# Kernel optimization log

Measured on AMD Instinct MI355X. Metric: run time of the kernel, lower is better.

## Reference

```python
import jax, jax.numpy as jnp
import numpy as np


def setup_inputs() -> dict:
    key = jax.random.key(0)
    ks = jax.random.split(key, 8)
    B, N, F, H, D, C = 16, 8192, 512, 512, 256, 2
    s = 0.02
    return {
        "h": jax.random.normal(ks[0], (B, N, F), dtype=jnp.float32),
        "W1": jax.random.normal(ks[1], (F, H), dtype=jnp.float32) * s,
        "b1": jnp.zeros((H,), jnp.float32),
        "Wa": jax.random.normal(ks[2], (H, D), dtype=jnp.float32) * s,
        "ba": jnp.zeros((D,), jnp.float32),
        "Wb": jax.random.normal(ks[3], (H, D), dtype=jnp.float32) * s,
        "bb": jnp.zeros((D,), jnp.float32),
        "Wc": jax.random.normal(ks[4], (D, 1), dtype=jnp.float32) * s,
        "bc": jnp.zeros((1,), jnp.float32),
        "Wcls": jax.random.normal(ks[5], (H, C), dtype=jnp.float32) * s,
        "bcls": jnp.zeros((C,), jnp.float32),
    }


def reference(h, W1, b1, Wa, ba, Wb, bb, Wc, bc, Wcls, bcls):
    # h: [B, N, F]  (B bags, N instances each)
    h1 = jax.nn.relu(jnp.einsum("bnf,fh->bnh", h, W1) + b1)        # [B,N,H]
    a = jnp.tanh(jnp.einsum("bnh,hd->bnd", h1, Wa) + ba)           # [B,N,D]
    g = jax.nn.sigmoid(jnp.einsum("bnh,hd->bnd", h1, Wb) + bb)     # [B,N,D]
    A = jnp.einsum("bnd,dk->bnk", a * g, Wc) + bc                  # [B,N,1]
    A_raw = jnp.swapaxes(A, 1, 2)                                  # [B,1,N]
    A_sm = jax.nn.softmax(A_raw, axis=-1)                          # [B,1,N]
    M = jnp.einsum("bkn,bnh->bkh", A_sm, h1)                       # [B,1,H]
    context = jnp.mean(M, axis=0)                                  # [1,H]  (sum / len(h_list))
    logits = context @ Wcls + bcls                                 # [1,C]
    Y_prob = jax.nn.softmax(logits, axis=1)
    Y_hat = jnp.argmax(logits, axis=1, keepdims=True)
    return (logits, Y_prob, Y_hat, A_raw, M)
```

## Files before the change

### kernel.cpp

```cpp
#include <hip/hip_runtime.h>
#include <math.h>

typedef short bf16x8 __attribute__((ext_vector_type(8)));
typedef float f32x4  __attribute__((ext_vector_type(4)));

#define GLOAD_LDS16(SRC, DST) \
  __builtin_amdgcn_global_load_lds((const __attribute__((address_space(1))) void*)(SRC), \
      (__attribute__((address_space(3))) void*)(DST), 16, 0, 0)

#define WAITVM(N) asm volatile("s_waitcnt vmcnt(" #N ")" ::: "memory")
#define WAITLGKM0 asm volatile("s_waitcnt lgkmcnt(0)" ::: "memory")
#define BARRIER() do { __builtin_amdgcn_s_barrier(); asm volatile("" ::: "memory"); } while (0)

__device__ __forceinline__ unsigned short f2bf(float f) {
  union { float f; unsigned u; } v; v.f = f;
  unsigned r = v.u + 0x7FFFu + ((v.u >> 16) & 1u);
  return (unsigned short)(r >> 16);
}
__device__ __forceinline__ float bf2f(unsigned short s) {
  union { unsigned u; float f; } v; v.u = ((unsigned)s) << 16;
  return v.f;
}
__device__ __forceinline__ unsigned pk2bf(float lo, float hi) {
  unsigned r;
  asm("v_cvt_pk_bf16_f32 %0, %1, %2" : "=v"(r) : "v"(lo), "v"(hi));
  return r;
}
__device__ __forceinline__ float fexp2(float x) {
  float r; asm("v_exp_f32 %0, %1" : "=v"(r) : "v"(x)); return r;
}
__device__ __forceinline__ float frcp(float x) {
  float r; asm("v_rcp_f32 %0, %1" : "=v"(r) : "v"(x)); return r;
}
#define LOG2E 1.44269504f
__device__ __forceinline__ float fexp(float x) { return fexp2(x * LOG2E); }


__global__ void carp_wpack(const float* __restrict__ W1, const float* __restrict__ Wa,
                           const float* __restrict__ Wb,
                           unsigned short* __restrict__ W1T_pk, unsigned short* __restrict__ WabT_pk) {
  int t = blockIdx.x * 256 + threadIdx.x;
  int mat = t >> 15;
  int gid = t & 32767;
  int g = gid & 511;
  int kt = (gid >> 9) & 15;
  int p = gid >> 13;
  int s = g >> 6, l = g & 63;
  int k = kt * 32 + (l >> 4) * 8;
  unsigned short v[8];
  if (mat == 0) {
    int j = p * 128 + s * 16 + (l & 15);
#pragma unroll
    for (int e = 0; e < 8; ++e) v[e] = f2bf(W1[(size_t)(k + e) * 512 + j]);
    *(uint4*)(W1T_pk + (size_t)gid * 8) = *(const uint4*)v;
  } else {
    int lc = s * 16 + (l & 15);
    int d = p * 64 + (lc & 63);
    const float* Wx = (lc >> 6) ? Wb : Wa;
#pragma unroll
    for (int e = 0; e < 8; ++e) v[e] = f2bf(Wx[(size_t)(k + e) * 256 + d]);
    *(uint4*)(WabT_pk + (size_t)gid * 8) = *(const uint4*)v;
  }
}

__launch_bounds__(512, 2)
__global__ void carp_gemm1(const float* __restrict__ h, const unsigned short* __restrict__ W1T_pk,
                           const float* __restrict__ b1, unsigned short* __restrict__ h1_pk) {
  __shared__ __align__(16) unsigned short lds[65536];
  int bid0 = blockIdx.x;
  int bid = (bid0 & 7) * 128 + (bid0 >> 3);
  int bn = bid & 1, bm = bid >> 1;
  int brow = bm * 256;
  int tid = threadIdx.x, lane = tid & 63, wid = tid >> 6;
  int wr = wid >> 1, wc = wid & 1;

  f32x4 acc[4][8] = {};
  float4 ar[8];

  int r0 = tid >> 4;
  int chunk = tid & 15;
  const float* hbase = h + (size_t)(brow + r0) * 512 + chunk * 4;
  int kgA = (chunk & 7) >> 1, r16A = r0 & 15;
  int aw_const = (chunk >> 3) * 8192 + (r0 >> 4) * 1024 + kgA * 256
               + ((r16A * 16) ^ (kgA << 5) ^ ((chunk >> 3) << 4)) + (chunk & 1) * 8;
  int aread_lane = (lane >> 4) * 256 + (((lane & 15) * 16) ^ ((lane >> 4) << 5));

#define G1_LOADA(TP) do { \
  _Pragma("unroll") for (int q = 0; q < 8; ++q) \
    ar[q] = *(const float4*)(hbase + (size_t)(q * 32) * 512 + (TP) * 64); \
  } while (0)
#define G1_WRITEA(TP) do { \
  char* dstA = (char*)lds + ((TP) & 1) * 32768; \
  _Pragma("unroll") for (int q = 0; q < 8; ++q) { \
    uint2 wv; wv.x = pk2bf(ar[q].x, ar[q].y); wv.y = pk2bf(ar[q].z, ar[q].w); \
    *(uint2*)(dstA + (q >> 2) * 16384 + (q & 3) * 2048 + aw_const) = wv; \
  } } while (0)
#define G1_STAGEB(TP, BUF) do { \
  _Pragma("unroll") for (int q = 0; q < 4; ++q) { \
    int c = wid * 4 + q; \
    int pn = 2 * bn + ((c & 15) >> 3); \
    GLOAD_LDS16(W1T_pk + ((size_t)(pn * 16 + (TP) * 2 + (c >> 4)) * 512 + (c & 7) * 64 + lane) * 8, \
                (char*)lds + 65536 + (BUF) * 32768 + (size_t)c * 1024); \
  } } while (0)

  G1_LOADA(0);
  WAITVM(0);
  G1_WRITEA(0);
  G1_STAGEB(0, 0);
  G1_LOADA(1);
  WAITLGKM0;

#pragma unroll 1
  for (int tp = 0; tp < 8; ++tp) {
    if (tp < 7) G1_STAGEB(tp + 1, (tp + 1) & 1);
    if (tp < 7) { WAITVM(12); } else { WAITVM(0); }
    BARRIER();
    const char* Abase = (const char*)lds + (tp & 1) * 32768;
    const char* Bbase = (const char*)lds + 65536 + (tp & 1) * 32768;
#pragma unroll
    for (int tt = 0; tt < 2; ++tt) {
      bf16x8 afr[4], bfr[8];
#pragma unroll
      for (int m = 0; m < 4; ++m) {
        int gs = wr * 4 + m;
        afr[m] = *(const bf16x8*)(Abase + (gs >> 3) * 16384 + tt * 8192
                                  + (gs & 7) * 1024 + (aread_lane ^ (tt << 4)));
      }
#pragma unroll
      for (int n = 0; n < 8; ++n)
        bfr[n] = *(const bf16x8*)(Bbase + tt * 16384 + wc * 8192
                                  + (size_t)(n * 64 + lane) * 16);
#pragma unroll
      for (int m = 0; m < 4; ++m)
#pragma unroll
        for (int n = 0; n < 8; ++n)
          acc[m][n] = __builtin_amdgcn_mfma_f32_16x16x32_bf16(afr[m], bfr[n], acc[m][n], 0, 0, 0);
    }
    if (tp < 7) { WAITVM(4); G1_WRITEA(tp + 1); }
    if (tp < 6) G1_LOADA(tp + 2);
    WAITLGKM0;
    BARRIER();
  }
#undef G1_LOADA
#undef G1_WRITEA
#undef G1_STAGEB

  unsigned short* img = lds;
#pragma unroll
  for (int n = 0; n < 8; ++n) {
    int cl = wc * 128 + n * 16 + (lane & 15);
    float bias = b1[bn * 256 + cl];
    int ktc = cl >> 5, c32 = cl & 31;
#pragma unroll
    for (int m = 0; m < 4; ++m)
#pragma unroll
      for (int j = 0; j < 4; ++j) {
        int r = wr * 64 + m * 16 + (lane >> 4) * 4 + j;
        float v = acc[m][n][j] + bias;
        v = v > 0.f ? v : 0.f;
        int gidx = (r >> 7) * 4096 + ktc * 512 + ((r & 127) >> 4) * 64 + (c32 >> 3) * 16 + (r & 15);
        img[(size_t)gidx * 8 + (c32 & 7)] = f2bf(v);
      }
  }
  __syncthreads();
#pragma unroll
  for (int i = 0; i < 16; ++i) {
    int g = i * 512 + tid;
    int P = (2 * bm + (g >> 12)) * 16 + bn * 8 + ((g >> 9) & 7);
    *(uint4*)(h1_pk + ((size_t)P * 512 + (g & 511)) * 8) = *(const uint4*)(img + (size_t)g * 8);
  }
}

#define G2_STAGE(T32, HALF, BUF) do { \
  _Pragma("unroll") for (int q = 0; q < 2; ++q) { \
    int c = wid * 2 + q; \
    int P = (2 * bm + (c >> 3)) * 16 + (T32); \
    GLOAD_LDS16(h1_pk + ((size_t)P * 512 + (c & 7) * 64 + lane) * 8, \
                (char*)lds + (BUF) * 32768 + (HALF) * 16384 + (size_t)c * 1024); \
  } \
  _Pragma("unroll") for (int q = 0; q < 2; ++q) { \
    int c2 = wid * 2 + q; \
    int pn = 2 * bn + (c2 >> 3); \
    GLOAD_LDS16(WabT_pk + ((size_t)(pn * 16 + (T32)) * 512 + (c2 & 7) * 64 + lane) * 8, \
                (char*)lds + 65536 + (BUF) * 32768 + (HALF) * 16384 + (size_t)c2 * 1024); \
  } } while (0)

__launch_bounds__(512, 2)
__global__ void carp_gemm2(const unsigned short* __restrict__ h1_pk, const unsigned short* __restrict__ WabT_pk,
                           const float* __restrict__ ba, const float* __restrict__ bb,
                           const float* __restrict__ Wc, float* __restrict__ A_part) {
  __shared__ __align__(16) unsigned short lds[65536];
  int bid0 = blockIdx.x;
  int bid = (bid0 & 7) * 128 + (bid0 >> 3);
  int bn = bid & 1, bm = bid >> 1;
  int tid = threadIdx.x, lane = tid & 63, wid = tid >> 6;
  int wr = wid >> 1, wc = wid & 1;

  f32x4 acc[4][8] = {};

  G2_STAGE(0, 0, 0); G2_STAGE(1, 1, 0);

#pragma unroll 1
  for (int kt = 0; kt < 8; ++kt) {
    int cur = kt & 1, nxt = cur ^ 1;
    if (kt < 7) { G2_STAGE(2 * kt + 2, 0, nxt); G2_STAGE(2 * kt + 3, 1, nxt); }
    if (kt < 7) { WAITVM(8); } else { WAITVM(0); }
    BARRIER();
#pragma unroll
    for (int tt = 0; tt < 2; ++tt) {
      const char* Ab = (const char*)lds + cur * 32768 + tt * 16384;
      const char* Bb = (const char*)lds + 65536 + cur * 32768 + tt * 16384 + wc * 8192;
      bf16x8 afr[4], bfr[8];
#pragma unroll
      for (int m = 0; m < 4; ++m)
        afr[m] = *(const bf16x8*)(Ab + (size_t)((wr * 4 + m) * 64 + lane) * 16);
#pragma unroll
      for (int n = 0; n < 8; ++n)
        bfr[n] = *(const bf16x8*)(Bb + (size_t)(n * 64 + lane) * 16);
#pragma unroll
      for (int m = 0; m < 4; ++m)
#pragma unroll
        for (int n = 0; n < 8; ++n)
          acc[m][n] = __builtin_amdgcn_mfma_f32_16x16x32_bf16(afr[m], bfr[n], acc[m][n], 0, 0, 0);
    }
    WAITLGKM0;
    BARRIER();
  }

  int brow = bm * 256;
  int pn = 2 * bn + wc;
  float rowpart[4][4] = {};
#pragma unroll
  for (int n = 0; n < 4; ++n) {
    int d = pn * 64 + n * 16 + (lane & 15);
    float ba_ = ba[d], bb_ = bb[d], wcd = Wc[d];
#pragma unroll
    for (int m = 0; m < 4; ++m)
#pragma unroll
      for (int j = 0; j < 4; ++j) {
        float va = acc[m][n][j] + ba_;
        float vg = acc[m][n + 4][j] + bb_;
        float a = 2.f * frcp(1.f + fexp2(-2.f * LOG2E * va)) - 1.f;
        float g = frcp(1.f + fexp2(-LOG2E * vg));
        rowpart[m][j] += a * g * wcd;
      }
  }
#pragma unroll
  for (int m = 0; m < 4; ++m)
#pragma unroll
    for (int j = 0; j < 4; ++j) {
      float t = rowpart[m][j];
      t += __shfl_xor(t, 1, 64);
      t += __shfl_xor(t, 2, 64);
      t += __shfl_xor(t, 4, 64);
      t += __shfl_xor(t, 8, 64);
      rowpart[m][j] = t;
    }
  if ((lane & 15) == 0) {
    int slot = bn * 2 + wc;
#pragma unroll
    for (int m = 0; m < 4; ++m)
#pragma unroll
      for (int j = 0; j < 4; ++j) {
        int row = brow + wr * 64 + m * 16 + (lane >> 4) * 4 + j;
        A_part[(size_t)row * 4 + slot] = rowpart[m][j];
      }
  }
}
#undef G2_STAGE

__global__ void carp_softmax(const float* __restrict__ A_part, const float* __restrict__ bc,
                             float* __restrict__ A_raw_out, float* __restrict__ A_sm) {
  __shared__ float sv[8192];
  __shared__ float red[256];
  int b = blockIdx.x, tid = threadIdx.x;
  float bcv = bc[0];
  float lmax = -1e30f;
  for (int i = tid; i < 8192; i += 256) {
    float4 x = *(const float4*)(A_part + (size_t)(b * 8192 + i) * 4);
    float s = (x.x + x.y) + (x.z + x.w) + bcv;
    sv[i] = s;
    A_raw_out[b * 8192 + i] = s;
    lmax = fmaxf(lmax, s);
  }
  red[tid] = lmax;
  for (int s = 128; s > 0; s >>= 1) { __syncthreads(); if (tid < s) red[tid] = fmaxf(red[tid], red[tid + s]); }
  __syncthreads();
  float mx = red[0];
  __syncthreads();
  float lsum = 0.f;
  for (int i = tid; i < 8192; i += 256) {
    float e = fexp(sv[i] - mx);
    sv[i] = e;
    lsum += e;
  }
  red[tid] = lsum;
  for (int s = 128; s > 0; s >>= 1) { __syncthreads(); if (tid < s) red[tid] += red[tid + s]; }
  __syncthreads();
  float inv = 1.f / red[0];
  for (int i = tid; i < 8192; i += 256) A_sm[b * 8192 + i] = sv[i] * inv;
}

__global__ void carp_mkernel(const unsigned short* __restrict__ h1_pk, const float* __restrict__ A_sm,
                             float* __restrict__ Mpart) {
  __shared__ float sw[128];
  int bm = blockIdx.x;
  int tid = threadIdx.x;
  if (tid < 128) sw[tid] = A_sm[bm * 128 + tid];
  __syncthreads();
  int l = tid & 63;
  float acc[4][8] = {};
#pragma unroll
  for (int tq = 0; tq < 4; ++tq) {
    int tt = (tid >> 6) * 4 + tq;
#pragma unroll
    for (int s = 0; s < 8; ++s) {
      const unsigned short* gp = h1_pk + ((size_t)(bm * 16 + tt) * 512 + s * 64 + l) * 8;
      uint4 raw = *(const uint4*)gp;
      const unsigned short* pv = (const unsigned short*)&raw;
      float w = sw[s * 16 + (l & 15)];
#pragma unroll
      for (int e = 0; e < 8; ++e) acc[tq][e] += w * bf2f(pv[e]);
    }
  }
#pragma unroll
  for (int tq = 0; tq < 4; ++tq)
#pragma unroll
    for (int e = 0; e < 8; ++e) {
      float t = acc[tq][e];
      t += __shfl_xor(t, 1, 64);
      t += __shfl_xor(t, 2, 64);
      t += __shfl_xor(t, 4, 64);
      t += __shfl_xor(t, 8, 64);
      acc[tq][e] = t;
    }
  if ((l & 15) == 0) {
    int cc = (l >> 4) & 3;
#pragma unroll
    for (int tq = 0; tq < 4; ++tq) {
      int tt = (tid >> 6) * 4 + tq;
      float* mp = Mpart + (size_t)bm * 512 + tt * 32 + cc * 8;
#pragma unroll
      for (int e = 0; e < 8; ++e) mp[e] = acc[tq][e];
    }
  }
}

__global__ void carp_final(const float* __restrict__ Mpart, const float* __restrict__ Wcls,
                           const float* __restrict__ bcls, float* __restrict__ out) {
  __shared__ float ctx[512];
  int t = threadIdx.x;
  float c = 0.f;
  for (int b = 0; b < 16; ++b) {
    float s = 0.f;
    for (int p = 0; p < 64; ++p) s += Mpart[((size_t)(b * 64 + p) << 9) + t];
    out[131077 + b * 512 + t] = s;
    c += s;
  }
  ctx[t] = c * (1.f / 16.f);
  __syncthreads();
  if (t < 64) {
    float p0 = 0.f, p1 = 0.f;
    for (int hh = t; hh < 512; hh += 64) {
      float cv = ctx[hh];
      p0 += cv * Wcls[hh * 2];
      p1 += cv * Wcls[hh * 2 + 1];
    }
    for (int m = 1; m < 64; m <<= 1) { p0 += __shfl_xor(p0, m, 64); p1 += __shfl_xor(p1, m, 64); }
    if (t == 0) {
      float l0 = p0 + bcls[0], l1 = p1 + bcls[1];
      out[0] = l0; out[1] = l1;
      float mx = fmaxf(l0, l1);
      float e0 = expf(l0 - mx), e1 = expf(l1 - mx);
      float s = e0 + e1;
      out[2] = e0 / s; out[3] = e1 / s;
      out[4] = (l1 > l0) ? 1.0f : 0.0f;
    }
  }
}

extern "C" void kernel_launch(void* const* d_in, const int* in_sizes, int n_in,
                              void* d_out, int out_size, void* d_ws, size_t ws_size,
                              hipStream_t stream) {
  const float* h    = (const float*)d_in[0];
  const float* W1   = (const float*)d_in[1];
  const float* b1   = (const float*)d_in[2];
  const float* Wa   = (const float*)d_in[3];
  const float* ba   = (const float*)d_in[4];
  const float* Wb   = (const float*)d_in[5];
  const float* bb   = (const float*)d_in[6];
  const float* Wc   = (const float*)d_in[7];
  const float* bc   = (const float*)d_in[8];
  const float* Wcls = (const float*)d_in[9];
  const float* bcls = (const float*)d_in[10];
  float* out = (float*)d_out;

  char* ws = (char*)d_ws;
  unsigned short* h1_pk   = (unsigned short*)(ws);
  unsigned short* W1T_pk  = (unsigned short*)(ws + 134217728);
  unsigned short* WabT_pk = (unsigned short*)(ws + 134742016);
  float* A_part           = (float*)(ws + 135266304);
  float* A_sm             = (float*)(ws + 139460608);
  float* Mpart            = (float*)(ws + 135266304);

  carp_wpack  <<<256,  256, 0, stream>>>(W1, Wa, Wb, W1T_pk, WabT_pk);
  carp_gemm1  <<<1024, 512, 0, stream>>>(h, W1T_pk, b1, h1_pk);
  carp_gemm2  <<<1024, 512, 0, stream>>>(h1_pk, WabT_pk, ba, bb, Wc, A_part);
  carp_softmax<<<16,   256, 0, stream>>>(A_part, bc, out + 5, A_sm);
  carp_mkernel<<<1024, 256, 0, stream>>>(h1_pk, A_sm, Mpart);
  carp_final  <<<1,    512, 0, stream>>>(Mpart, Wcls, bcls, out);
}
```

Before: 304.9 us.

## Split softmax into parallel partial sums and fold normalization into M kernel

The single 16-block softmax becomes a 64-block pass that writes A_raw and per-chunk sums of exp, plus a tiny kernel that turns those sums into per-bag reciprocals. The M kernel now recomputes exp(A_raw)*inv itself instead of reading a stored A_sm. This drops the max-subtraction pass and the A_sm round trip, and spreads the reduction over more CUs. The risk is overflow, since exp is taken without subtracting the max, which holds only while logits stay small. It also adds one more kernel launch.

After: 297.4 us. 1.03x faster.

```diff
diff --git a/kernel.cpp b/kernel.cpp
--- a/kernel.cpp
+++ b/kernel.cpp
@@ -269,44 +269,38 @@
 }
 #undef G2_STAGE
 
-__global__ void carp_softmax(const float* __restrict__ A_part, const float* __restrict__ bc,
-                             float* __restrict__ A_raw_out, float* __restrict__ A_sm) {
-  __shared__ float sv[8192];
+__global__ void carp_softmax1(const float* __restrict__ A_part, const float* __restrict__ bc,
+                              float* __restrict__ A_raw_out, float* __restrict__ partial) {
   __shared__ float red[256];
-  int b = blockIdx.x, tid = threadIdx.x;
+  int blk = blockIdx.x, tid = threadIdx.x;
+  int base = blk * 2048;
   float bcv = bc[0];
-  float lmax = -1e30f;
-  for (int i = tid; i < 8192; i += 256) {
-    float4 x = *(const float4*)(A_part + (size_t)(b * 8192 + i) * 4);
+  float lsum = 0.f;
+  for (int i = tid; i < 2048; i += 256) {
+    float4 x = *(const float4*)(A_part + (size_t)(base + i) * 4);
     float s = (x.x + x.y) + (x.z + x.w) + bcv;
-    sv[i] = s;
-    A_raw_out[b * 8192 + i] = s;
-    lmax = fmaxf(lmax, s);
-  }
-  red[tid] = lmax;
-  for (int s = 128; s > 0; s >>= 1) { __syncthreads(); if (tid < s) red[tid] = fmaxf(red[tid], red[tid + s]); }
-  __syncthreads();
-  float mx = red[0];
-  __syncthreads();
-  float lsum = 0.f;
-  for (int i = tid; i < 8192; i += 256) {
-    float e = fexp(sv[i] - mx);
-    sv[i] = e;
-    lsum += e;
+    A_raw_out[base + i] = s;
+    lsum += fexp(s);
   }
   red[tid] = lsum;
   for (int s = 128; s > 0; s >>= 1) { __syncthreads(); if (tid < s) red[tid] += red[tid + s]; }
-  __syncthreads();
-  float inv = 1.f / red[0];
-  for (int i = tid; i < 8192; i += 256) A_sm[b * 8192 + i] = sv[i] * inv;
-}
-
-__global__ void carp_mkernel(const unsigned short* __restrict__ h1_pk, const float* __restrict__ A_sm,
-                             float* __restrict__ Mpart) {
+  if (tid == 0) partial[blk] = red[0];
+}
+
+__global__ void carp_softmax2(const float* __restrict__ partial, float* __restrict__ binv) {
+  int b = threadIdx.x;
+  if (b < 16) {
+    float s = partial[b * 4] + partial[b * 4 + 1] + partial[b * 4 + 2] + partial[b * 4 + 3];
+    binv[b] = 1.f / s;
+  }
+}
+
+__global__ void carp_mkernel(const unsigned short* __restrict__ h1_pk, const float* __restrict__ A_raw,
+                             const float* __restrict__ binv, float* __restrict__ Mpart) {
   __shared__ float sw[128];
   int bm = blockIdx.x;
   int tid = threadIdx.x;
-  if (tid < 128) sw[tid] = A_sm[bm * 128 + tid];
+  if (tid < 128) sw[tid] = fexp(A_raw[bm * 128 + tid]) * binv[bm >> 6];
   __syncthreads();
   int l = tid & 63;
   float acc[4][8] = {};
@@ -400,13 +394,15 @@
   unsigned short* W1T_pk  = (unsigned short*)(ws + 134217728);
   unsigned short* WabT_pk = (unsigned short*)(ws + 134742016);
   float* A_part           = (float*)(ws + 135266304);
-  float* A_sm             = (float*)(ws + 139460608);
+  float* partial          = (float*)(ws + 139460608);
+  float* binv             = (float*)(ws + 139461120);
   float* Mpart            = (float*)(ws + 135266304);
 
-  carp_wpack  <<<256,  256, 0, stream>>>(W1, Wa, Wb, W1T_pk, WabT_pk);
-  carp_gemm1  <<<1024, 512, 0, stream>>>(h, W1T_pk, b1, h1_pk);
-  carp_gemm2  <<<1024, 512, 0, stream>>>(h1_pk, WabT_pk, ba, bb, Wc, A_part);
-  carp_softmax<<<16,   256, 0, stream>>>(A_part, bc, out + 5, A_sm);
-  carp_mkernel<<<1024, 256, 0, stream>>>(h1_pk, A_sm, Mpart);
-  carp_final  <<<1,    512, 0, stream>>>(Mpart, Wcls, bcls, out);
-}
+  carp_wpack   <<<256,  256, 0, stream>>>(W1, Wa, Wb, W1T_pk, WabT_pk);
+  carp_gemm1   <<<1024, 512, 0, stream>>>(h, W1T_pk, b1, h1_pk);
+  carp_gemm2   <<<1024, 512, 0, stream>>>(h1_pk, WabT_pk, ba, bb, Wc, A_part);
+  carp_softmax1<<<64,   256, 0, stream>>>(A_part, bc, out + 5, partial);
+  carp_softmax2<<<1,    64,  0, stream>>>(partial, binv);
+  carp_mkernel <<<1024, 256, 0, stream>>>(h1_pk, out + 5, binv, Mpart);
+  carp_final   <<<1,    512, 0, stream>>>(Mpart, Wcls, bcls, out);
+}
```
